# Optimization experiments

Measured on AMD Instinct MI355X. Metric: run time of the kernel, lower is better.

## Reference

```python
import jax, jax.numpy as jnp
import numpy as np

N_NODE = 50000
D_FEAT = 128
N_EDGE = 625000
SIM_THRESH = 0.1


def setup_inputs() -> dict:
    key = jax.random.key(0)
    k1, k2, k3, k4, k5 = jax.random.split(key, 5)
    features = jax.random.normal(k1, (N_NODE, D_FEAT), dtype=jnp.float32)
    edge_weight = jax.random.uniform(k2, (N_EDGE,), dtype=jnp.float32)
    gate = jax.random.uniform(k3, (1,), dtype=jnp.float32)
    row = jax.random.randint(k4, (N_EDGE,), 0, N_NODE)
    col = jax.random.randint(k5, (N_EDGE,), 0, N_NODE)
    # avoid self-loops so the original's att[0,0]==0 / diagonal-removal branches
    # behave as the common (no self-loop) path
    col = jnp.where(col == row, (col + 1) % N_NODE, col)
    edge_index = jnp.stack([row, col], axis=0).astype(jnp.int64)
    return {"edge_index": edge_index, "edge_weight": edge_weight,
            "features": features, "gate": gate}


def reference(edge_index, edge_weight, features, gate):
    n_node = features.shape[0]
    row, col = edge_index[0], edge_index[1]
    # per-edge cosine similarity via normalized feature gather
    nrm = jnp.maximum(jnp.linalg.norm(features, axis=1, keepdims=True), 1e-12)
    fn = features / nrm
    sim = jnp.sum(fn[row] * fn[col], axis=1)            # [E]
    sim = jnp.where(sim < SIM_THRESH, 0.0, sim)         # threshold (all remaining >= 0.1)
    # row-wise L1 normalize over the sparse adjacency
    row_sum = jax.ops.segment_sum(jnp.abs(sim), row, num_segments=n_node)  # [N]
    denom = jnp.where(row_sum > 0, row_sum, 1.0)
    sim_norm = sim / denom[row]
    # degree-based self-loop weight lam = 1/(deg+1); only affects diagonal edges
    degree = jax.ops.segment_sum((sim_norm != 0).astype(sim_norm.dtype), row,
                                 num_segments=n_node)
    lam = 1.0 / (degree + 1.0)
    att_edge = sim_norm + jnp.where(row == col, lam[row], 0.0)
    att_edge = jnp.exp(att_edge)
    # learnable gate blend + clamp
    out = gate[0] * edge_weight + (1.0 - gate[0]) * att_edge
    return jnp.maximum(out, 0.0)
```

## Files before the change

kernel.cpp:

```cpp
#include <hip/hip_runtime.h>
#include <hip/hip_fp16.h>
#include <math.h>

#define N_NODE 50000
#define D_FEAT 128
#define N_EDGE 625000
#define SIM_THRESH 0.1f
#define SCREEN_LO 0.08f
#define BAND_EPS 5e-4f

typedef float v2f __attribute__((ext_vector_type(2)));
typedef int   v4i __attribute__((ext_vector_type(4)));
typedef float v4f __attribute__((ext_vector_type(4)));

#if __has_builtin(__builtin_amdgcn_sdot4)
#define USE_SDOT4 1
#else
#define USE_SDOT4 0
#endif

#if __has_builtin(__builtin_amdgcn_fdot2)
#define USE_FDOT2 1
typedef _Float16 h2v __attribute__((ext_vector_type(2)));
#else
#define USE_FDOT2 0
#endif

__global__ void prep_kernel(const float* __restrict__ feat,
                            float* __restrict__ inv_nrm,
                            __half* __restrict__ fn16,
                            unsigned int* __restrict__ qtab,
                            float* __restrict__ row_sum,
                            float* __restrict__ degree) {
    int g = blockIdx.x * blockDim.x + threadIdx.x;
    if (g < N_NODE) { row_sum[g] = 0.0f; degree[g] = 0.0f; }
    int node = g >> 5;
    int lane = g & 31;
    if (node >= N_NODE) return;
    float4 v = ((const float4*)(feat + (size_t)node * D_FEAT))[lane];
    float ss = v.x * v.x + v.y * v.y + v.z * v.z + v.w * v.w;
#pragma unroll
    for (int o = 16; o > 0; o >>= 1) ss += __shfl_xor(ss, o, 32);
    float inv = 1.0f / fmaxf(sqrtf(ss), 1e-12f);
    if (lane == 0) inv_nrm[node] = inv;
    float x0 = v.x * inv, x1 = v.y * inv, x2 = v.z * inv, x3 = v.w * inv;
    __half2 h0 = __floats2half2_rn(x0, x1);
    __half2 h1 = __floats2half2_rn(x2, x3);
    uint2 p;
    p.x = *(unsigned int*)&h0;
    p.y = *(unsigned int*)&h1;
    ((uint2*)(fn16 + (size_t)node * D_FEAT))[lane] = p;
#if USE_SDOT4
    int q0 = (int)rintf(x0 * 127.0f);
    int q1 = (int)rintf(x1 * 127.0f);
    int q2 = (int)rintf(x2 * 127.0f);
    int q3 = (int)rintf(x3 * 127.0f);
    unsigned int w = (unsigned int)(q0 & 0xff) | ((unsigned int)(q1 & 0xff) << 8) |
                     ((unsigned int)(q2 & 0xff) << 16) | ((unsigned int)(q3 & 0xff) << 24);
#else
    int wi = __builtin_amdgcn_cvt_pk_fp8_f32(x0, x1, 0, false);
    wi = __builtin_amdgcn_cvt_pk_fp8_f32(x2, x3, wi, true);
    unsigned int w = (unsigned int)wi;
#endif
    qtab[(size_t)node * 32 + lane] = w;
}

__global__ __launch_bounds__(256)
void edge_sim8_kernel(const int* __restrict__ row,
                      const int* __restrict__ col,
                      const float* __restrict__ feat,
                      const float* __restrict__ inv_nrm,
                      const __half* __restrict__ fn16,
                      const unsigned int* __restrict__ qtab,
                      float* __restrict__ sim_out,
                      float* __restrict__ row_sum,
                      float* __restrict__ degree) {
    int g = blockIdx.x * blockDim.x + threadIdx.x;
    int edge = g >> 3;
    int lane = g & 7;
    if (edge >= N_EDGE) return;
    int r = __builtin_nontemporal_load(row + edge);
    int c = __builtin_nontemporal_load(col + edge);

    uint4 aw = ((const uint4*)(qtab + (size_t)r * 32))[lane];
    uint4 bw = ((const uint4*)(qtab + (size_t)c * 32))[lane];
    float d;
#if USE_SDOT4
    {
        const unsigned int* awp = (const unsigned int*)&aw;
        const unsigned int* bwp = (const unsigned int*)&bw;
        int acc = 0;
#pragma unroll
        for (int i = 0; i < 4; i++)
            acc = __builtin_amdgcn_sdot4((int)awp[i], (int)bwp[i], acc, false);
#pragma unroll
        for (int o = 4; o > 0; o >>= 1) acc += __shfl_xor(acc, o, 8);
        d = (float)acc * (1.0f / 16129.0f);
    }
#else
    {
        const unsigned int* awp = (const unsigned int*)&aw;
        const unsigned int* bwp = (const unsigned int*)&bw;
        d = 0.0f;
#pragma unroll
        for (int i = 0; i < 4; i++) {
            v2f alo = __builtin_amdgcn_cvt_pk_f32_fp8((int)awp[i], false);
            v2f ahi = __builtin_amdgcn_cvt_pk_f32_fp8((int)awp[i], true);
            v2f blo = __builtin_amdgcn_cvt_pk_f32_fp8((int)bwp[i], false);
            v2f bhi = __builtin_amdgcn_cvt_pk_f32_fp8((int)bwp[i], true);
            d = fmaf(alo.x, blo.x, d); d = fmaf(alo.y, blo.y, d);
            d = fmaf(ahi.x, bhi.x, d); d = fmaf(ahi.y, bhi.y, d);
        }
#pragma unroll
        for (int o = 4; o > 0; o >>= 1) d += __shfl_xor(d, o, 8);
    }
#endif

    float s = 0.0f;
    if (d > SCREEN_LO) {
        const float4* ar = (const float4*)(fn16 + (size_t)r * D_FEAT);
        const float4* br = (const float4*)(fn16 + (size_t)c * D_FEAT);
        float4 a0 = ar[lane], a1 = ar[lane + 8];
        float4 b0 = br[lane], b1 = br[lane + 8];
        float dh = 0.0f;
#if USE_FDOT2
        {
            const h2v* ah0 = (const h2v*)&a0;
            const h2v* bh0 = (const h2v*)&b0;
            const h2v* ah1 = (const h2v*)&a1;
            const h2v* bh1 = (const h2v*)&b1;
#pragma unroll
            for (int i = 0; i < 4; i++) {
                dh = __builtin_amdgcn_fdot2(ah0[i], bh0[i], dh, false);
                dh = __builtin_amdgcn_fdot2(ah1[i], bh1[i], dh, false);
            }
        }
#else
        {
            const __half2* ah0 = (const __half2*)&a0;
            const __half2* bh0 = (const __half2*)&b0;
            const __half2* ah1 = (const __half2*)&a1;
            const __half2* bh1 = (const __half2*)&b1;
#pragma unroll
            for (int i = 0; i < 4; i++) {
                float2 afv = __half22float2(ah0[i]);
                float2 bfv = __half22float2(bh0[i]);
                dh = fmaf(afv.x, bfv.x, dh);
                dh = fmaf(afv.y, bfv.y, dh);
                float2 afw = __half22float2(ah1[i]);
                float2 bfw = __half22float2(bh1[i]);
                dh = fmaf(afw.x, bfw.x, dh);
                dh = fmaf(afw.y, bfw.y, dh);
            }
        }
#endif
#pragma unroll
        for (int o = 4; o > 0; o >>= 1) dh += __shfl_xor(dh, o, 8);
        if (fabsf(dh - SIM_THRESH) < BAND_EPS) {
            const float4* fr = (const float4*)(feat + (size_t)r * D_FEAT);
            const float4* fc = (const float4*)(feat + (size_t)c * D_FEAT);
            float dd = 0.0f;
#pragma unroll
            for (int q = 0; q < 4; q++) {
                float4 av = fr[lane + q * 8];
                float4 bv = fc[lane + q * 8];
                dd += av.x * bv.x + av.y * bv.y + av.z * bv.z + av.w * bv.w;
            }
#pragma unroll
            for (int o = 4; o > 0; o >>= 1) dd += __shfl_xor(dd, o, 8);
            dh = dd * inv_nrm[r] * inv_nrm[c];
        }
        s = (dh < SIM_THRESH) ? 0.0f : dh;
    }
    if (lane == 0) {
        sim_out[edge] = s;
        if (s != 0.0f) {
            atomicAdd(&row_sum[r], s);
            atomicAdd(&degree[r], 1.0f);
        }
    }
}

__global__ void edge_out_kernel(const int* __restrict__ row,
                                const int* __restrict__ col,
                                const float* __restrict__ sim,
                                const float* __restrict__ row_sum,
                                const float* __restrict__ degree,
                                const float* __restrict__ ew,
                                const float* __restrict__ gate,
                                float* __restrict__ out) {
    int t = blockIdx.x * blockDim.x + threadIdx.x;
    if (t >= N_EDGE / 4) return;
    v4i r4 = __builtin_nontemporal_load((const v4i*)row + t);
    v4i c4 = __builtin_nontemporal_load((const v4i*)col + t);
    v4f s4 = __builtin_nontemporal_load((const v4f*)sim + t);
    v4f w4 = __builtin_nontemporal_load((const v4f*)ew + t);
    float gv = gate[0];
    float og = 1.0f - gv;
    v4f o4;
#pragma unroll
    for (int i = 0; i < 4; i++) {
        int   ri = r4[i];
        float rs = row_sum[ri];
        float att = s4[i] / ((rs > 0.0f) ? rs : 1.0f);
        if (ri == c4[i]) att += 1.0f / (degree[ri] + 1.0f);
        o4[i] = fmaxf(gv * w4[i] + og * expf(att), 0.0f);
    }
    __builtin_nontemporal_store(o4, (v4f*)out + t);
}

__global__ void inv_norm_kernel(const float* __restrict__ feat,
                                float* __restrict__ inv_nrm,
                                float* __restrict__ row_sum,
                                float* __restrict__ degree) {
    int g = blockIdx.x * blockDim.x + threadIdx.x;
    if (g < N_NODE) { row_sum[g] = 0.0f; degree[g] = 0.0f; }
    int node = g >> 5;
    int lane = g & 31;
    if (node >= N_NODE) return;
    float4 v = ((const float4*)(feat + (size_t)node * D_FEAT))[lane];
    float ss = v.x * v.x + v.y * v.y + v.z * v.z + v.w * v.w;
#pragma unroll
    for (int o = 16; o > 0; o >>= 1) ss += __shfl_down(ss, o, 32);
    if (lane == 0) inv_nrm[node] = 1.0f / fmaxf(sqrtf(ss), 1e-12f);
}

__global__ void edge_sim_kernel(const int* __restrict__ row,
                                const int* __restrict__ col,
                                const float* __restrict__ feat,
                                const float* __restrict__ inv_nrm,
                                float* __restrict__ sim_out,
                                float* __restrict__ row_sum,
                                float* __restrict__ degree) {
    int g = blockIdx.x * blockDim.x + threadIdx.x;
    int edge = g >> 5;
    int lane = g & 31;
    if (edge >= N_EDGE) return;
    int r = row[edge];
    int c = col[edge];
    float4 a = ((const float4*)(feat + (size_t)r * D_FEAT))[lane];
    float4 b = ((const float4*)(feat + (size_t)c * D_FEAT))[lane];
    float d = a.x * b.x + a.y * b.y + a.z * b.z + a.w * b.w;
#pragma unroll
    for (int o = 16; o > 0; o >>= 1) d += __shfl_down(d, o, 32);
    if (lane == 0) {
        float s = d * inv_nrm[r] * inv_nrm[c];
        if (s < SIM_THRESH) s = 0.0f;
        sim_out[edge] = s;
        if (s != 0.0f) {
            atomicAdd(&row_sum[r], s);
            atomicAdd(&degree[r], 1.0f);
        }
    }
}

extern "C" void kernel_launch(void* const* d_in, const int* in_sizes, int n_in,
                              void* d_out, int out_size, void* d_ws, size_t ws_size,
                              hipStream_t stream) {
    const int*   edge_index = (const int*)d_in[0];
    const float* ew         = (const float*)d_in[1];
    const float* feat       = (const float*)d_in[2];
    const float* gate       = (const float*)d_in[3];
    float*       out        = (float*)d_out;

    const int* row = edge_index;
    const int* col = edge_index + N_EDGE;

    float* row_sum = (float*)d_ws;
    float* degree  = row_sum + N_NODE;
    float* inv_nrm = degree + N_NODE;
    float* sim     = inv_nrm + N_NODE;
    __half* fn16   = (__half*)(sim + N_EDGE);
    unsigned int* qtab = (unsigned int*)(fn16 + (size_t)N_NODE * D_FEAT);

    size_t need = (size_t)(3 * N_NODE + N_EDGE) * 4
                + (size_t)N_NODE * D_FEAT * 2
                + (size_t)N_NODE * D_FEAT;

    const int block = 256;

    if (ws_size >= need) {
        {
            long long threads = (long long)N_NODE * 32;
            prep_kernel<<<(int)((threads + block - 1) / block), block, 0, stream>>>(
                feat, inv_nrm, fn16, qtab, row_sum, degree);
        }
        {
            long long threads = (long long)N_EDGE * 8;
            edge_sim8_kernel<<<(int)((threads + block - 1) / block), block, 0, stream>>>(
                row, col, feat, inv_nrm, fn16, qtab, sim, row_sum, degree);
        }
        {
            int threads = N_EDGE / 4;
            edge_out_kernel<<<(threads + block - 1) / block, block, 0, stream>>>(
                row, col, sim, row_sum, degree, ew, gate, out);
        }
    } else {
        {
            long long threads = (long long)N_NODE * 32;
            inv_norm_kernel<<<(int)((threads + block - 1) / block), block, 0, stream>>>(
                feat, inv_nrm, row_sum, degree);
        }
        {
            long long threads = (long long)N_EDGE * 32;
            edge_sim_kernel<<<(int)((threads + block - 1) / block), block, 0, stream>>>(
                row, col, feat, inv_nrm, sim, row_sum, degree);
        }
        {
            int threads = N_EDGE / 4;
            edge_out_kernel<<<(threads + block - 1) / block, block, 0, stream>>>(
                row, col, sim, row_sum, degree, ew, gate, out);
        }
    }
}
```

Before: 127.3 us.

## Process four edges per 8-lane group with batched gathers and branch-free fp16 refinement

Result: no change. 126.4 us (-0.7%).

```diff
diff --git a/kernel.cpp b/kernel.cpp
--- a/kernel.cpp
+++ b/kernel.cpp
@@ -76,107 +76,235 @@
                       float* __restrict__ row_sum,
                       float* __restrict__ degree) {
     int g = blockIdx.x * blockDim.x + threadIdx.x;
-    int edge = g >> 3;
+    int grp = g >> 3;
     int lane = g & 7;
-    if (edge >= N_EDGE) return;
-    int r = __builtin_nontemporal_load(row + edge);
-    int c = __builtin_nontemporal_load(col + edge);
-
-    uint4 aw = ((const uint4*)(qtab + (size_t)r * 32))[lane];
-    uint4 bw = ((const uint4*)(qtab + (size_t)c * 32))[lane];
-    float d;
+    if (grp >= N_EDGE / 4) return;
+    size_t e0 = (size_t)grp * 4;
+
+    int idx = __builtin_nontemporal_load(
+        row + (size_t)(lane >> 2) * N_EDGE + e0 + (lane & 3));
+    int r0 = __shfl(idx, 0, 8), r1 = __shfl(idx, 1, 8);
+    int r2 = __shfl(idx, 2, 8), r3 = __shfl(idx, 3, 8);
+    int c0 = __shfl(idx, 4, 8), c1 = __shfl(idx, 5, 8);
+    int c2 = __shfl(idx, 6, 8), c3 = __shfl(idx, 7, 8);
+
+    const uint4* q = (const uint4*)qtab;
+    uint4 aw0 = q[(size_t)r0 * 8 + lane];
+    uint4 aw1 = q[(size_t)r1 * 8 + lane];
+    uint4 aw2 = q[(size_t)r2 * 8 + lane];
+    uint4 aw3 = q[(size_t)r3 * 8 + lane];
+    uint4 bw0 = q[(size_t)c0 * 8 + lane];
+    uint4 bw1 = q[(size_t)c1 * 8 + lane];
+    uint4 bw2 = q[(size_t)c2 * 8 + lane];
+    uint4 bw3 = q[(size_t)c3 * 8 + lane];
+
+    float d0, d1, d2, d3;
 #if USE_SDOT4
     {
-        const unsigned int* awp = (const unsigned int*)&aw;
-        const unsigned int* bwp = (const unsigned int*)&bw;
-        int acc = 0;
-#pragma unroll
-        for (int i = 0; i < 4; i++)
-            acc = __builtin_amdgcn_sdot4((int)awp[i], (int)bwp[i], acc, false);
-#pragma unroll
-        for (int o = 4; o > 0; o >>= 1) acc += __shfl_xor(acc, o, 8);
-        d = (float)acc * (1.0f / 16129.0f);
+        int a0 = 0, a1 = 0, a2 = 0, a3 = 0;
+        a0 = __builtin_amdgcn_sdot4((int)aw0.x, (int)bw0.x, a0, false);
+        a1 = __builtin_amdgcn_sdot4((int)aw1.x, (int)bw1.x, a1, false);
+        a2 = __builtin_amdgcn_sdot4((int)aw2.x, (int)bw2.x, a2, false);
+        a3 = __builtin_amdgcn_sdot4((int)aw3.x, (int)bw3.x, a3, false);
+        a0 = __builtin_amdgcn_sdot4((int)aw0.y, (int)bw0.y, a0, false);
+        a1 = __builtin_amdgcn_sdot4((int)aw1.y, (int)bw1.y, a1, false);
+        a2 = __builtin_amdgcn_sdot4((int)aw2.y, (int)bw2.y, a2, false);
+        a3 = __builtin_amdgcn_sdot4((int)aw3.y, (int)bw3.y, a3, false);
+        a0 = __builtin_amdgcn_sdot4((int)aw0.z, (int)bw0.z, a0, false);
+        a1 = __builtin_amdgcn_sdot4((int)aw1.z, (int)bw1.z, a1, false);
+        a2 = __builtin_amdgcn_sdot4((int)aw2.z, (int)bw2.z, a2, false);
+        a3 = __builtin_amdgcn_sdot4((int)aw3.z, (int)bw3.z, a3, false);
+        a0 = __builtin_amdgcn_sdot4((int)aw0.w, (int)bw0.w, a0, false);
+        a1 = __builtin_amdgcn_sdot4((int)aw1.w, (int)bw1.w, a1, false);
+        a2 = __builtin_amdgcn_sdot4((int)aw2.w, (int)bw2.w, a2, false);
+        a3 = __builtin_amdgcn_sdot4((int)aw3.w, (int)bw3.w, a3, false);
+#pragma unroll
+        for (int o = 4; o > 0; o >>= 1) {
+            a0 += __shfl_xor(a0, o, 8);
+            a1 += __shfl_xor(a1, o, 8);
+            a2 += __shfl_xor(a2, o, 8);
+            a3 += __shfl_xor(a3, o, 8);
+        }
+        d0 = (float)a0 * (1.0f / 16129.0f);
+        d1 = (float)a1 * (1.0f / 16129.0f);
+        d2 = (float)a2 * (1.0f / 16129.0f);
+        d3 = (float)a3 * (1.0f / 16129.0f);
     }
 #else
     {
-        const unsigned int* awp = (const unsigned int*)&aw;
-        const unsigned int* bwp = (const unsigned int*)&bw;
-        d = 0.0f;
+        float f0 = 0.f, f1 = 0.f, f2 = 0.f, f3 = 0.f;
+        const unsigned int* ap0 = (const unsigned int*)&aw0;
+        const unsigned int* bp0 = (const unsigned int*)&bw0;
+        const unsigned int* ap1 = (const unsigned int*)&aw1;
+        const unsigned int* bp1 = (const unsigned int*)&bw1;
+        const unsigned int* ap2 = (const unsigned int*)&aw2;
+        const unsigned int* bp2 = (const unsigned int*)&bw2;
+        const unsigned int* ap3 = (const unsigned int*)&aw3;
+        const unsigned int* bp3 = (const unsigned int*)&bw3;
 #pragma unroll
         for (int i = 0; i < 4; i++) {
-            v2f alo = __builtin_amdgcn_cvt_pk_f32_fp8((int)awp[i], false);
-            v2f ahi = __builtin_amdgcn_cvt_pk_f32_fp8((int)awp[i], true);
-            v2f blo = __builtin_amdgcn_cvt_pk_f32_fp8((int)bwp[i], false);
-            v2f bhi = __builtin_amdgcn_cvt_pk_f32_fp8((int)bwp[i], true);
-            d = fmaf(alo.x, blo.x, d); d = fmaf(alo.y, blo.y, d);
-            d = fmaf(ahi.x, bhi.x, d); d = fmaf(ahi.y, bhi.y, d);
-        }
-#pragma unroll
-        for (int o = 4; o > 0; o >>= 1) d += __shfl_xor(d, o, 8);
+            v2f x, y;
+            x = __builtin_amdgcn_cvt_pk_f32_fp8((int)ap0[i], false);
+            y = __builtin_amdgcn_cvt_pk_f32_fp8((int)bp0[i], false);
+            f0 = fmaf(x.x, y.x, f0); f0 = fmaf(x.y, y.y, f0);
+            x = __builtin_amdgcn_cvt_pk_f32_fp8((int)ap0[i], true);
+            y = __builtin_amdgcn_cvt_pk_f32_fp8((int)bp0[i], true);
+            f0 = fmaf(x.x, y.x, f0); f0 = fmaf(x.y, y.y, f0);
+            x = __builtin_amdgcn_cvt_pk_f32_fp8((int)ap1[i], false);
+            y = __builtin_amdgcn_cvt_pk_f32_fp8((int)bp1[i], false);
+            f1 = fmaf(x.x, y.x, f1); f1 = fmaf(x.y, y.y, f1);
+            x = __builtin_amdgcn_cvt_pk_f32_fp8((int)ap1[i], true);
+            y = __builtin_amdgcn_cvt_pk_f32_fp8((int)bp1[i], true);
+            f1 = fmaf(x.x, y.x, f1); f1 = fmaf(x.y, y.y, f1);
+            x = __builtin_amdgcn_cvt_pk_f32_fp8((int)ap2[i], false);
+            y = __builtin_amdgcn_cvt_pk_f32_fp8((int)bp2[i], false);
+            f2 = fmaf(x.x, y.x, f2); f2 = fmaf(x.y, y.y, f2);
+            x = __builtin_amdgcn_cvt_pk_f32_fp8((int)ap2[i], true);
+            y = __builtin_amdgcn_cvt_pk_f32_fp8((int)bp2[i], true);
+            f2 = fmaf(x.x, y.x, f2); f2 = fmaf(x.y, y.y, f2);
+            x = __builtin_amdgcn_cvt_pk_f32_fp8((int)ap3[i], false);
+            y = __builtin_amdgcn_cvt_pk_f32_fp8((int)bp3[i], false);
+            f3 = fmaf(x.x, y.x, f3); f3 = fmaf(x.y, y.y, f3);
+            x = __builtin_amdgcn_cvt_pk_f32_fp8((int)ap3[i], true);
+            y = __builtin_amdgcn_cvt_pk_f32_fp8((int)bp3[i], true);
+            f3 = fmaf(x.x, y.x, f3); f3 = fmaf(x.y, y.y, f3);
+        }
+#pragma unroll
+        for (int o = 4; o > 0; o >>= 1) {
+            f0 += __shfl_xor(f0, o, 8);
+            f1 += __shfl_xor(f1, o, 8);
+            f2 += __shfl_xor(f2, o, 8);
+            f3 += __shfl_xor(f3, o, 8);
+        }
+        d0 = f0; d1 = f1; d2 = f2; d3 = f3;
     }
 #endif
-
-    float s = 0.0f;
-    if (d > SCREEN_LO) {
-        const float4* ar = (const float4*)(fn16 + (size_t)r * D_FEAT);
-        const float4* br = (const float4*)(fn16 + (size_t)c * D_FEAT);
-        float4 a0 = ar[lane], a1 = ar[lane + 8];
-        float4 b0 = br[lane], b1 = br[lane + 8];
-        float dh = 0.0f;
+    bool p0 = d0 > SCREEN_LO, p1 = d1 > SCREEN_LO;
+    bool p2 = d2 > SCREEN_LO, p3 = d3 > SCREEN_LO;
+
+    int ra0 = p0 ? r0 : 0, rb0 = p0 ? c0 : 0;
+    int ra1 = p1 ? r1 : 0, rb1 = p1 ? c1 : 0;
+    int ra2 = p2 ? r2 : 0, rb2 = p2 ? c2 : 0;
+    int ra3 = p3 ? r3 : 0, rb3 = p3 ? c3 : 0;
+    const v4f* f16 = (const v4f*)fn16;
+    v4f A00 = f16[(size_t)ra0 * 16 + lane];
+    v4f A01 = f16[(size_t)ra0 * 16 + lane + 8];
+    v4f B00 = f16[(size_t)rb0 * 16 + lane];
+    v4f B01 = f16[(size_t)rb0 * 16 + lane + 8];
+    v4f A10 = f16[(size_t)ra1 * 16 + lane];
+    v4f A11 = f16[(size_t)ra1 * 16 + lane + 8];
+    v4f B10 = f16[(size_t)rb1 * 16 + lane];
+    v4f B11 = f16[(size_t)rb1 * 16 + lane + 8];
+    v4f A20 = f16[(size_t)ra2 * 16 + lane];
+    v4f A21 = f16[(size_t)ra2 * 16 + lane + 8];
+    v4f B20 = f16[(size_t)rb2 * 16 + lane];
+    v4f B21 = f16[(size_t)rb2 * 16 + lane + 8];
+    v4f A30 = f16[(size_t)ra3 * 16 + lane];
+    v4f A31 = f16[(size_t)ra3 * 16 + lane + 8];
+    v4f B30 = f16[(size_t)rb3 * 16 + lane];
+    v4f B31 = f16[(size_t)rb3 * 16 + lane + 8];
+
+    float dh0 = 0.f, dh1 = 0.f, dh2 = 0.f, dh3 = 0.f;
 #if USE_FDOT2
-        {
-            const h2v* ah0 = (const h2v*)&a0;
-            const h2v* bh0 = (const h2v*)&b0;
-            const h2v* ah1 = (const h2v*)&a1;
-            const h2v* bh1 = (const h2v*)&b1;
-#pragma unroll
-            for (int i = 0; i < 4; i++) {
-                dh = __builtin_amdgcn_fdot2(ah0[i], bh0[i], dh, false);
-                dh = __builtin_amdgcn_fdot2(ah1[i], bh1[i], dh, false);
-            }
-        }
+#define DOT16(acc, X, Y)                                                     \
+    {                                                                        \
+        const h2v* xp = (const h2v*)&(X);                                    \
+        const h2v* yp = (const h2v*)&(Y);                                    \
+        acc = __builtin_amdgcn_fdot2(xp[0], yp[0], acc, false);              \
+        acc = __builtin_amdgcn_fdot2(xp[1], yp[1], acc, false);              \
+        acc = __builtin_amdgcn_fdot2(xp[2], yp[2], acc, false);              \
+        acc = __builtin_amdgcn_fdot2(xp[3], yp[3], acc, false);              \
+    }
 #else
-        {
-            const __half2* ah0 = (const __half2*)&a0;
-            const __half2* bh0 = (const __half2*)&b0;
-            const __half2* ah1 = (const __half2*)&a1;
-            const __half2* bh1 = (const __half2*)&b1;
-#pragma unroll
-            for (int i = 0; i < 4; i++) {
-                float2 afv = __half22float2(ah0[i]);
-                float2 bfv = __half22float2(bh0[i]);
-                dh = fmaf(afv.x, bfv.x, dh);
-                dh = fmaf(afv.y, bfv.y, dh);
-                float2 afw = __half22float2(ah1[i]);
-                float2 bfw = __half22float2(bh1[i]);
-                dh = fmaf(afw.x, bfw.x, dh);
-                dh = fmaf(afw.y, bfw.y, dh);
-            }
-        }
+#define DOT16(acc, X, Y)                                                     \
+    {                                                                        \
+        const __half2* xp = (const __half2*)&(X);                            \
+        const __half2* yp = (const __half2*)&(Y);                            \
+        for (int i_ = 0; i_ < 4; i_++) {                                     \
+            float2 xa = __half22float2(xp[i_]);                              \
+            float2 ya = __half22float2(yp[i_]);                              \
+            acc = fmaf(xa.x, ya.x, acc);                                     \
+            acc = fmaf(xa.y, ya.y, acc);                                     \
+        }                                                                    \
+    }
 #endif
-#pragma unroll
-        for (int o = 4; o > 0; o >>= 1) dh += __shfl_xor(dh, o, 8);
-        if (fabsf(dh - SIM_THRESH) < BAND_EPS) {
-            const float4* fr = (const float4*)(feat + (size_t)r * D_FEAT);
-            const float4* fc = (const float4*)(feat + (size_t)c * D_FEAT);
-            float dd = 0.0f;
-#pragma unroll
-            for (int q = 0; q < 4; q++) {
-                float4 av = fr[lane + q * 8];
-                float4 bv = fc[lane + q * 8];
-                dd += av.x * bv.x + av.y * bv.y + av.z * bv.z + av.w * bv.w;
-            }
-#pragma unroll
-            for (int o = 4; o > 0; o >>= 1) dd += __shfl_xor(dd, o, 8);
-            dh = dd * inv_nrm[r] * inv_nrm[c];
-        }
-        s = (dh < SIM_THRESH) ? 0.0f : dh;
-    }
-    if (lane == 0) {
-        sim_out[edge] = s;
-        if (s != 0.0f) {
-            atomicAdd(&row_sum[r], s);
-            atomicAdd(&degree[r], 1.0f);
+    DOT16(dh0, A00, B00) DOT16(dh0, A01, B01)
+    DOT16(dh1, A10, B10) DOT16(dh1, A11, B11)
+    DOT16(dh2, A20, B20) DOT16(dh2, A21, B21)
+    DOT16(dh3, A30, B30) DOT16(dh3, A31, B31)
+#pragma unroll
+    for (int o = 4; o > 0; o >>= 1) {
+        dh0 += __shfl_xor(dh0, o, 8);
+        dh1 += __shfl_xor(dh1, o, 8);
+        dh2 += __shfl_xor(dh2, o, 8);
+        dh3 += __shfl_xor(dh3, o, 8);
+    }
+
+    if (p0 && fabsf(dh0 - SIM_THRESH) < BAND_EPS) {
+        const v4f* fr = (const v4f*)(feat + (size_t)r0 * D_FEAT);
+        const v4f* fc = (const v4f*)(feat + (size_t)c0 * D_FEAT);
+        float dd = 0.0f;
+#pragma unroll
+        for (int qq = 0; qq < 4; qq++) {
+            v4f av = fr[lane + qq * 8], bv = fc[lane + qq * 8];
+            dd += av.x * bv.x + av.y * bv.y + av.z * bv.z + av.w * bv.w;
+        }
+#pragma unroll
+        for (int o = 4; o > 0; o >>= 1) dd += __shfl_xor(dd, o, 8);
+        dh0 = dd * inv_nrm[r0] * inv_nrm[c0];
+    }
+    if (p1 && fabsf(dh1 - SIM_THRESH) < BAND_EPS) {
+        const v4f* fr = (const v4f*)(feat + (size_t)r1 * D_FEAT);
+        const v4f* fc = (const v4f*)(feat + (size_t)c1 * D_FEAT);
+        float dd = 0.0f;
+#pragma unroll
+        for (int qq = 0; qq < 4; qq++) {
+            v4f av = fr[lane + qq * 8], bv = fc[lane + qq * 8];
+            dd += av.x * bv.x + av.y * bv.y + av.z * bv.z + av.w * bv.w;
+        }
+#pragma unroll
+        for (int o = 4; o > 0; o >>= 1) dd += __shfl_xor(dd, o, 8);
+        dh1 = dd * inv_nrm[r1] * inv_nrm[c1];
+    }
+    if (p2 && fabsf(dh2 - SIM_THRESH) < BAND_EPS) {
+        const v4f* fr = (const v4f*)(feat + (size_t)r2 * D_FEAT);
+        const v4f* fc = (const v4f*)(feat + (size_t)c2 * D_FEAT);
+        float dd = 0.0f;
+#pragma unroll
+        for (int qq = 0; qq < 4; qq++) {
+            v4f av = fr[lane + qq * 8], bv = fc[lane + qq * 8];
+            dd += av.x * bv.x + av.y * bv.y + av.z * bv.z + av.w * bv.w;
+        }
+#pragma unroll
+        for (int o = 4; o > 0; o >>= 1) dd += __shfl_xor(dd, o, 8);
+        dh2 = dd * inv_nrm[r2] * inv_nrm[c2];
+    }
+    if (p3 && fabsf(dh3 - SIM_THRESH) < BAND_EPS) {
+        const v4f* fr = (const v4f*)(feat + (size_t)r3 * D_FEAT);
+        const v4f* fc = (const v4f*)(feat + (size_t)c3 * D_FEAT);
+        float dd = 0.0f;
+#pragma unroll
+        for (int qq = 0; qq < 4; qq++) {
+            v4f av = fr[lane + qq * 8], bv = fc[lane + qq * 8];
+            dd += av.x * bv.x + av.y * bv.y + av.z * bv.z + av.w * bv.w;
+        }
+#pragma unroll
+        for (int o = 4; o > 0; o >>= 1) dd += __shfl_xor(dd, o, 8);
+        dh3 = dd * inv_nrm[r3] * inv_nrm[c3];
+    }
+
+    float s0 = (p0 && dh0 >= SIM_THRESH) ? dh0 : 0.0f;
+    float s1 = (p1 && dh1 >= SIM_THRESH) ? dh1 : 0.0f;
+    float s2 = (p2 && dh2 >= SIM_THRESH) ? dh2 : 0.0f;
+    float s3 = (p3 && dh3 >= SIM_THRESH) ? dh3 : 0.0f;
+
+    if (lane < 4) {
+        float sv = (lane == 0) ? s0 : (lane == 1) ? s1 : (lane == 2) ? s2 : s3;
+        int   rv = (lane == 0) ? r0 : (lane == 1) ? r1 : (lane == 2) ? r2 : r3;
+        sim_out[e0 + lane] = sv;
+        if (sv != 0.0f) {
+            atomicAdd(&row_sum[rv], sv);
+            atomicAdd(&degree[rv], 1.0f);
         }
     }
 }
@@ -286,7 +414,7 @@
                 feat, inv_nrm, fn16, qtab, row_sum, degree);
         }
         {
-            long long threads = (long long)N_EDGE * 8;
+            long long threads = (long long)(N_EDGE / 4) * 8;
             edge_sim8_kernel<<<(int)((threads + block - 1) / block), block, 0, stream>>>(
                 row, col, feat, inv_nrm, fn16, qtab, sim, row_sum, degree);
         }
```
